# Kernel optimization log

Measured on AMD Instinct MI355X. Metric: run time of the kernel, lower is better.

## Reference

```python
import jax, jax.numpy as jnp
import numpy as np

B, S, H = 8, 4096, 1152
GRID = 64  # 64x64 patch grid, pooled 4x4 -> 256 tokens
OUT_LEN = 256


def setup_inputs() -> dict:
    key = jax.random.key(0)
    k1, k2, k3 = jax.random.split(key, 3)
    x = jax.random.normal(k1, (B, S, H), dtype=jnp.float32)
    std_bias = jax.random.normal(k2, (H,), dtype=jnp.float32)
    std_scale = jax.random.uniform(k3, (H,), dtype=jnp.float32)
    idx = jnp.arange(S, dtype=jnp.int32)
    cols = idx % GRID
    rows = idx // GRID
    pos = jnp.stack([cols, rows], axis=-1)  # [S, 2] (x, y) patch coords
    position_ids = jnp.broadcast_to(pos, (B, S, 2))
    return {
        "x": x,
        "std_bias": std_bias,
        "std_scale": std_scale,
        "position_ids": position_ids,
        "image_output_length": OUT_LEN,
    }


def reference(x, std_bias, std_scale, position_ids, image_output_length):
    b, s, h = x.shape
    out_len = int(image_output_length)
    if out_len > s:
        raise ValueError("cannot pool")
    if s != out_len:
        k = int((s // out_len) ** 0.5)
        assert k * k * out_len == s
        # bin each patch coordinate into a kxk pooling window
        max_x = position_ids[..., 0].max(axis=-1, keepdims=True) + 1  # [B,1]
        kidx = position_ids // k  # [B,S,2]
        seg = kidx[..., 0] + (max_x // k) * kidx[..., 1]  # [B,S] in [0, out_len)
        # scatter-mean instead of one-hot matmul (same math)
        flat_seg = (seg + jnp.arange(b, dtype=seg.dtype)[:, None] * out_len).reshape(-1)
        pooled = jax.ops.segment_sum(x.reshape(b * s, h), flat_seg, num_segments=b * out_len)
        x = pooled.reshape(b, out_len, h) * (1.0 / (k * k))
    x = x * jnp.float32(np.sqrt(h))
    x = (x - std_bias) * std_scale
    return x.astype(jnp.float32)
```

## Files before the change

kernel.cpp:

```cpp
#include <hip/hip_runtime.h>

#define B 8
#define S 4096
#define H 1152
#define OUT 256
#define KP 4
#define CAP 16
#define H4 (H / 4)

#define WS_COUNTS 0
#define WS_LISTS  (B * OUT)

__global__ __launch_bounds__(1024) void build_index_kernel(
    const int* __restrict__ pos, int* __restrict__ ws) {
    const int b = blockIdx.x;
    const int tid = threadIdx.x;

    __shared__ int s_max;
    __shared__ int s_cnt[OUT];
    __shared__ int s_lst[OUT][CAP];

    if (tid < OUT) s_cnt[tid] = 0;
    if (tid == 0) s_max = 0;

    int px[4], py[4];
    int mymax = 0;
    #pragma unroll
    for (int j = 0; j < 4; ++j) {
        const int s = tid + j * 1024;
        const int2 p = reinterpret_cast<const int2*>(pos)[b * S + s];
        px[j] = p.x; py[j] = p.y;
        mymax = mymax > p.x ? mymax : p.x;
    }
    #pragma unroll
    for (int off = 32; off > 0; off >>= 1) {
        const int o = __shfl_down(mymax, off, 64);
        mymax = mymax > o ? mymax : o;
    }
    __syncthreads();
    if ((tid & 63) == 0) atomicMax(&s_max, mymax);
    __syncthreads();

    const int mxk = (s_max + 1) / KP;
    #pragma unroll
    for (int j = 0; j < 4; ++j) {
        const int s = tid + j * 1024;
        const int seg = px[j] / KP + mxk * (py[j] / KP);
        const int slot = atomicAdd(&s_cnt[seg], 1);
        if (slot < CAP) s_lst[seg][slot] = s;
    }
    __syncthreads();

    if (tid < OUT) ws[WS_COUNTS + b * OUT + tid] = s_cnt[tid];
    for (int i = tid; i < OUT * CAP; i += 1024) {
        const int seg = i / CAP, slot = i % CAP;
        ws[WS_LISTS + (b * OUT + seg) * CAP + slot] = s_lst[seg][slot];
    }
}

__global__ __launch_bounds__(576) void pool_kernel(
    const float* __restrict__ x, const float* __restrict__ bias,
    const float* __restrict__ scale, const int* __restrict__ ws,
    float* __restrict__ out) {
    const int tp = blockIdx.x;
    const int tid = threadIdx.x;

    __shared__ int s_lst[2][CAP];
    __shared__ int s_cnt[2];

    if (tid < 2) {
        int c = ws[WS_COUNTS + tp * 2 + tid];
        s_cnt[tid] = c > CAP ? CAP : c;
    }
    if (tid >= 64 && tid < 64 + CAP)
        s_lst[0][tid - 64] = ws[WS_LISTS + (tp * 2) * CAP + (tid - 64)];
    else if (tid >= 128 && tid < 128 + CAP)
        s_lst[1][tid - 128] = ws[WS_LISTS + (tp * 2 + 1) * CAP + (tid - 128)];
    __syncthreads();

    const int k  = tid >= H4 ? 1 : 0;
    const int h4 = tid - k * H4;
    const int bt = tp * 2 + k;
    const int b  = bt >> 8;
    const int cnt = s_cnt[k];
    const float* xp = x + (size_t)b * S * H + (size_t)h4 * 4;

    float4 acc = make_float4(0.f, 0.f, 0.f, 0.f);
    if (cnt == CAP) {
        #pragma unroll
        for (int i = 0; i < CAP; ++i) {
            const float4 v = *reinterpret_cast<const float4*>(xp + (size_t)s_lst[k][i] * H);
            acc.x += v.x; acc.y += v.y; acc.z += v.z; acc.w += v.w;
        }
    } else {
        for (int i = 0; i < cnt; ++i) {
            const float4 v = *reinterpret_cast<const float4*>(xp + (size_t)s_lst[k][i] * H);
            acc.x += v.x; acc.y += v.y; acc.z += v.z; acc.w += v.w;
        }
    }

    const float mul = sqrtf((float)H) * (1.0f / (KP * KP));
    const float4 bs = *reinterpret_cast<const float4*>(bias + h4 * 4);
    const float4 sc = *reinterpret_cast<const float4*>(scale + h4 * 4);
    float4 r;
    r.x = (acc.x * mul - bs.x) * sc.x;
    r.y = (acc.y * mul - bs.y) * sc.y;
    r.z = (acc.z * mul - bs.z) * sc.z;
    r.w = (acc.w * mul - bs.w) * sc.w;
    *reinterpret_cast<float4*>(out + (size_t)bt * H + (size_t)h4 * 4) = r;
}

extern "C" void kernel_launch(void* const* d_in, const int* in_sizes, int n_in,
                              void* d_out, int out_size, void* d_ws, size_t ws_size,
                              hipStream_t stream) {
    const float* x         = (const float*)d_in[0];
    const float* std_bias  = (const float*)d_in[1];
    const float* std_scale = (const float*)d_in[2];
    const int*   pos       = (const int*)d_in[3];
    float* out = (float*)d_out;
    int* ws = (int*)d_ws;

    build_index_kernel<<<B, 1024, 0, stream>>>(pos, ws);
    pool_kernel<<<B * OUT / 2, 576, 0, stream>>>(x, std_bias, std_scale, ws, out);
}
```

Baseline: 32.89 us.

## Fuse index build into pooling kernel, each block scanning positions for its segments

Removes the separate index-building kernel and workspace. Each pooling block now reads all position ids of its batch, computes the max x coordinate, and builds member lists only for its own two segments before gathering. This eliminates a launch and the workspace write/read dependency, but makes every block redundantly scan the full position array.

```diff
diff --git a/kernel.cpp b/kernel.cpp
--- a/kernel.cpp
+++ b/kernel.cpp
@@ -7,30 +7,35 @@
 #define KP 4
 #define CAP 16
 #define H4 (H / 4)
+#define NT 576
+#define PPT 8
 
-#define WS_COUNTS 0
-#define WS_LISTS  (B * OUT)
-
-__global__ __launch_bounds__(1024) void build_index_kernel(
-    const int* __restrict__ pos, int* __restrict__ ws) {
-    const int b = blockIdx.x;
+__global__ __launch_bounds__(NT) void fused_pool_kernel(
+    const float* __restrict__ x, const float* __restrict__ bias,
+    const float* __restrict__ scale, const int* __restrict__ pos,
+    float* __restrict__ out) {
+    const int tp  = blockIdx.x;
     const int tid = threadIdx.x;
+    const int b   = tp >> 7;
+    const int seg0 = (tp * 2) & 255;
 
     __shared__ int s_max;
-    __shared__ int s_cnt[OUT];
-    __shared__ int s_lst[OUT][CAP];
+    __shared__ int s_cnt[2];
+    __shared__ int s_lst[2][CAP];
 
-    if (tid < OUT) s_cnt[tid] = 0;
     if (tid == 0) s_max = 0;
+    if (tid < 2) s_cnt[tid] = 0;
 
-    int px[4], py[4];
+    int px[PPT], py[PPT];
     int mymax = 0;
     #pragma unroll
-    for (int j = 0; j < 4; ++j) {
-        const int s = tid + j * 1024;
-        const int2 p = reinterpret_cast<const int2*>(pos)[b * S + s];
-        px[j] = p.x; py[j] = p.y;
-        mymax = mymax > p.x ? mymax : p.x;
+    for (int j = 0; j < PPT; ++j) {
+        const int s = tid + j * NT;
+        if (s < S) {
+            const int2 p = reinterpret_cast<const int2*>(pos)[b * S + s];
+            px[j] = p.x; py[j] = p.y;
+            mymax = mymax > p.x ? mymax : p.x;
+        } else { px[j] = -1; py[j] = 0; }
     }
     #pragma unroll
     for (int off = 32; off > 0; off >>= 1) {
@@ -40,49 +45,26 @@
     __syncthreads();
     if ((tid & 63) == 0) atomicMax(&s_max, mymax);
     __syncthreads();
+    const int mxk = (s_max + 1) / KP;
 
-    const int mxk = (s_max + 1) / KP;
     #pragma unroll
-    for (int j = 0; j < 4; ++j) {
-        const int s = tid + j * 1024;
-        const int seg = px[j] / KP + mxk * (py[j] / KP);
-        const int slot = atomicAdd(&s_cnt[seg], 1);
-        if (slot < CAP) s_lst[seg][slot] = s;
+    for (int j = 0; j < PPT; ++j) {
+        if (px[j] >= 0) {
+            const int seg = px[j] / KP + mxk * (py[j] / KP);
+            const int k = seg - seg0;
+            if (k == 0 || k == 1) {
+                const int slot = atomicAdd(&s_cnt[k], 1);
+                if (slot < CAP) s_lst[k][slot] = tid + j * NT;
+            }
+        }
     }
-    __syncthreads();
-
-    if (tid < OUT) ws[WS_COUNTS + b * OUT + tid] = s_cnt[tid];
-    for (int i = tid; i < OUT * CAP; i += 1024) {
-        const int seg = i / CAP, slot = i % CAP;
-        ws[WS_LISTS + (b * OUT + seg) * CAP + slot] = s_lst[seg][slot];
-    }
-}
-
-__global__ __launch_bounds__(576) void pool_kernel(
-    const float* __restrict__ x, const float* __restrict__ bias,
-    const float* __restrict__ scale, const int* __restrict__ ws,
-    float* __restrict__ out) {
-    const int tp = blockIdx.x;
-    const int tid = threadIdx.x;
-
-    __shared__ int s_lst[2][CAP];
-    __shared__ int s_cnt[2];
-
-    if (tid < 2) {
-        int c = ws[WS_COUNTS + tp * 2 + tid];
-        s_cnt[tid] = c > CAP ? CAP : c;
-    }
-    if (tid >= 64 && tid < 64 + CAP)
-        s_lst[0][tid - 64] = ws[WS_LISTS + (tp * 2) * CAP + (tid - 64)];
-    else if (tid >= 128 && tid < 128 + CAP)
-        s_lst[1][tid - 128] = ws[WS_LISTS + (tp * 2 + 1) * CAP + (tid - 128)];
     __syncthreads();
 
     const int k  = tid >= H4 ? 1 : 0;
     const int h4 = tid - k * H4;
     const int bt = tp * 2 + k;
-    const int b  = bt >> 8;
-    const int cnt = s_cnt[k];
+    int cnt = s_cnt[k];
+    if (cnt > CAP) cnt = CAP;
     const float* xp = x + (size_t)b * S * H + (size_t)h4 * 4;
 
     float4 acc = make_float4(0.f, 0.f, 0.f, 0.f);
@@ -118,8 +100,6 @@
     const float* std_scale = (const float*)d_in[2];
     const int*   pos       = (const int*)d_in[3];
     float* out = (float*)d_out;
-    int* ws = (int*)d_ws;
 
-    build_index_kernel<<<B, 1024, 0, stream>>>(pos, ws);
-    pool_kernel<<<B * OUT / 2, 576, 0, stream>>>(x, std_bias, std_scale, ws, out);
+    fused_pool_kernel<<<B * OUT / 2, NT, 0, stream>>>(x, std_bias, std_scale, pos, out);
 }
```

Result: faster. 31.11 us (-5.4%).
